# Performance work log

Measured on AMD Instinct MI355X. Metric: run time of the kernel, lower is better.

## Reference

```python
import jax, jax.numpy as jnp
import numpy as np


def setup_inputs() -> dict:
    key = jax.random.key(0)
    k1, k2 = jax.random.split(key)
    input_tensor = jax.random.normal(k1, (32, 128, 64, 64), dtype=jnp.float32)
    weights = jax.random.normal(k2, (256, 128, 3, 3), dtype=jnp.float32) * 0.05
    return {"input_tensor": input_tensor, "weights": weights}


def reference(input_tensor, weights):
    # Valid-padding, stride-1, no-bias direct conv2d (NCHW x OIHW -> NCHW),
    # identical math to the quintuple-loop slice*weight sum in the original.
    return jax.lax.conv_general_dilated(
        input_tensor,
        weights,
        window_strides=(1, 1),
        padding="VALID",
        dimension_numbers=("NCHW", "OIHW", "NCHW"),
    )
```

## Files before the change

kernel.cpp:

```cpp
#include <hip/hip_runtime.h>
#include <hip/hip_bf16.h>

#define N_IMG 32
#define CIN   128
#define INH   64
#define INW   64
#define COUT  256
#define OH    62
#define OW    62

typedef short          bf16x8 __attribute__((ext_vector_type(8)));
typedef unsigned short u16x8  __attribute__((ext_vector_type(8)));
typedef float          f32x4  __attribute__((ext_vector_type(4)));

__device__ __forceinline__ unsigned short f2bf(float x) {
    unsigned int u = __float_as_uint(x);
    u += 0x7fffu + ((u >> 16) & 1u);
    return (unsigned short)(u >> 16);
}

__global__ void wt_transform_kernel(const float* __restrict__ Wsrc,
                                    unsigned short* __restrict__ WT) {
    int idx = blockIdx.x * 256 + threadIdx.x;
    int i   = idx & 7;
    int co  = (idx >> 3) & 255;
    int cgk = idx >> 11;
    int cg  = cgk & 15;
    int khw = cgk >> 4;
    int kh  = khw / 3, kw = khw - 3 * kh;
    int ci  = cg * 8 + i;
    WT[idx] = f2bf(Wsrc[co * (CIN * 9) + ci * 9 + kh * 3 + kw]);
}

__global__ __launch_bounds__(256, 2)
void conv_mfma_kernel(const float* __restrict__ In,
                      const unsigned short* __restrict__ WT,
                      float* __restrict__ Out) {
    __shared__ unsigned short Lin[66 * 32];

    const int oh   = blockIdx.x;
    const int img  = blockIdx.y;
    const int tid  = threadIdx.x;
    const int wave = tid >> 6;
    const int lane = tid & 63;
    const int q    = lane >> 4;
    const int ml   = lane & 15;
    const int co_base = wave * 64;

    f32x4 acc[4][4];
    const f32x4 zero = {0.f, 0.f, 0.f, 0.f};
#pragma unroll
    for (int a = 0; a < 4; ++a)
#pragma unroll
        for (int b = 0; b < 4; ++b) acc[a][b] = zero;

    if (tid < 32) ((unsigned int*)&Lin[64 * 32])[tid] = 0u;

    const int s_iw = tid & 63;
    const int s_cg = tid >> 6;
    const bf16x8* WTv = (const bf16x8*)WT;

    for (int kh = 0; kh < 3; ++kh) {
        const int ih = oh + kh;
        for (int cb = 0; cb < 4; ++cb) {
            const float* p = In + (((img * CIN + cb * 32 + s_cg * 8) * INH + ih) * INW + s_iw);
            u16x8 v;
#pragma unroll
            for (int i = 0; i < 8; ++i) v[i] = f2bf(p[i * (INH * INW)]);
            __syncthreads();
            *(u16x8*)&Lin[s_iw * 32 + ((s_cg ^ (s_iw & 3)) << 3)] = v;
            __syncthreads();

#pragma unroll
            for (int kw = 0; kw < 3; ++kw) {
                const int khw = kh * 3 + kw;
                bf16x8 wf[4], xf[4];
#pragma unroll
                for (int mi = 0; mi < 4; ++mi)
                    wf[mi] = WTv[(khw * 16 + cb * 4 + q) * 256 + co_base + mi * 16 + ml];
#pragma unroll
                for (int ni = 0; ni < 4; ++ni) {
                    const int row = ni * 16 + ml + kw;
                    xf[ni] = *(const bf16x8*)&Lin[row * 32 + ((q ^ (row & 3)) << 3)];
                }
#pragma unroll
                for (int mi = 0; mi < 4; ++mi)
#pragma unroll
                    for (int ni = 0; ni < 4; ++ni)
                        acc[mi][ni] = __builtin_amdgcn_mfma_f32_16x16x32_bf16(
                            wf[mi], xf[ni], acc[mi][ni], 0, 0, 0);
            }
        }
    }

#pragma unroll
    for (int mi = 0; mi < 4; ++mi) {
#pragma unroll
        for (int r = 0; r < 4; ++r) {
            const int co = co_base + mi * 16 + q * 4 + r;
            float* op = Out + ((img * COUT + co) * OH + oh) * OW;
#pragma unroll
            for (int ni = 0; ni < 4; ++ni) {
                const int ow = ni * 16 + ml;
                if (ow < OW) op[ow] = acc[mi][ni][r];
            }
        }
    }
}

__global__ void conv_naive_kernel(const float* __restrict__ In,
                                  const float* __restrict__ Wt,
                                  float* __restrict__ Out) {
    int idx = blockIdx.x * 256 + threadIdx.x;
    const int total = N_IMG * COUT * OH * OW;
    if (idx >= total) return;
    int ow = idx % OW; int t = idx / OW;
    int oh = t % OH;   t /= OH;
    int co = t % COUT; int img = t / COUT;
    float s = 0.f;
    for (int ci = 0; ci < CIN; ++ci)
#pragma unroll
        for (int kh = 0; kh < 3; ++kh)
#pragma unroll
            for (int kw = 0; kw < 3; ++kw)
                s += In[((img * CIN + ci) * INH + oh + kh) * INW + ow + kw] *
                     Wt[co * CIN * 9 + ci * 9 + kh * 3 + kw];
    Out[idx] = s;
}

extern "C" void kernel_launch(void* const* d_in, const int* in_sizes, int n_in,
                              void* d_out, int out_size, void* d_ws, size_t ws_size,
                              hipStream_t stream) {
    const float* In   = (const float*)d_in[0];
    const float* Wsrc = (const float*)d_in[1];
    float* Out        = (float*)d_out;

    const size_t WT_BYTES = (size_t)9 * 16 * 256 * 8 * sizeof(unsigned short);
    if (ws_size >= WT_BYTES) {
        unsigned short* WT = (unsigned short*)d_ws;
        wt_transform_kernel<<<dim3(294912 / 256), dim3(256), 0, stream>>>(Wsrc, WT);
        conv_mfma_kernel<<<dim3(OH, N_IMG), dim3(256), 0, stream>>>(In, WT, Out);
    } else {
        const int total = N_IMG * COUT * OH * OW;
        conv_naive_kernel<<<dim3((total + 255) / 256), dim3(256), 0, stream>>>(In, Wsrc, Out);
    }
}
```

Baseline: 240.5 us.

## Pre-convert input to swizzled bf16 and double-buffer it into LDS via direct loads

Adds a separate kernel that converts the fp32 NCHW input once into a bf16, channel-blocked, XOR-swizzled layout in workspace. The conv kernel then streams rows straight into LDS with global_load_lds, double-buffered so the next stage loads while MFMAs run on the current one. It also halves threads per block, giving each wave 128 output channels, and remaps block ids to spread work. The aim is to remove repeated fp32 loads and conversions of each input row from the main loop and to hide load latency. The cost is an extra kernel launch and a full-tensor bf16 write and read through workspace, plus a path that only runs when the workspace is large enough.

```diff
diff --git a/kernel.cpp b/kernel.cpp
--- a/kernel.cpp
+++ b/kernel.cpp
@@ -17,6 +17,12 @@
     unsigned int u = __float_as_uint(x);
     u += 0x7fffu + ((u >> 16) & 1u);
     return (unsigned short)(u >> 16);
+}
+
+__device__ __forceinline__ void gload_lds16(const void* g, void* l) {
+    __builtin_amdgcn_global_load_lds(
+        (const __attribute__((address_space(1))) unsigned int*)g,
+        (__attribute__((address_space(3))) unsigned int*)l, 16, 0, 0);
 }
 
 __global__ void wt_transform_kernel(const float* __restrict__ Wsrc,
@@ -32,10 +38,121 @@
     WT[idx] = f2bf(Wsrc[co * (CIN * 9) + ci * 9 + kh * 3 + kw]);
 }
 
+__global__ __launch_bounds__(256)
+void in_transform_kernel(const float* __restrict__ In,
+                         unsigned short* __restrict__ TIn) {
+    const int bid = blockIdx.x;
+    const int ih  = bid & 63;
+    const int cb  = (bid >> 6) & 3;
+    const int img = bid >> 8;
+    const int c   = threadIdx.x;
+    const int iw  = c >> 2;
+    const int cg  = (c & 3) ^ ((iw >> 1) & 3);
+    const float* p = In + ((img * CIN + cb * 32 + cg * 8) * INH + ih) * INW + iw;
+    u16x8 v;
+#pragma unroll
+    for (int i = 0; i < 8; ++i) v[i] = f2bf(p[i * (INH * INW)]);
+    *(u16x8*)&TIn[(bid * 256 + c) * 8] = v;
+}
+
+__global__ __launch_bounds__(128, 2)
+void conv_mfma_bf16_kernel(const unsigned short* __restrict__ TIn,
+                           const unsigned short* __restrict__ WT,
+                           float* __restrict__ Out) {
+    __shared__ unsigned short Lin[2][2112];
+
+    const int g   = blockIdx.x;
+    const int f   = (g & 7) * 248 + (g >> 3);
+    const int img = f / OH;
+    const int oh  = f - img * OH;
+
+    const int tid  = threadIdx.x;
+    const int wave = tid >> 6;
+    const int lane = tid & 63;
+    const int q    = lane >> 4;
+    const int ml   = lane & 15;
+    const int co_base = wave * 128;
+
+    const unsigned short* tin_base = TIn + (size_t)img * (4 * 64 * 2048);
+    const bf16x8* WTv = (const bf16x8*)WT;
+    const int wlane = q * 256 + co_base + ml;
+
+    int xoff[3][4];
+#pragma unroll
+    for (int kw = 0; kw < 3; ++kw)
+#pragma unroll
+        for (int ni = 0; ni < 4; ++ni) {
+            const int r = ni * 16 + ml + kw;
+            xoff[kw][ni] = r * 32 + ((q ^ ((r >> 1) & 3)) << 3);
+        }
+
+    f32x4 acc[8][4];
+    const f32x4 zero = {0.f, 0.f, 0.f, 0.f};
+#pragma unroll
+    for (int a = 0; a < 8; ++a)
+#pragma unroll
+        for (int b = 0; b < 4; ++b) acc[a][b] = zero;
+
+    {
+        const unsigned short* src = tin_base + (oh) * 2048;
+        gload_lds16(src + (wave * 64 + lane) * 8, &Lin[0][wave * 512]);
+        gload_lds16(src + (128 + wave * 64 + lane) * 8, &Lin[0][1024 + wave * 512]);
+    }
+    if (tid < 64) ((unsigned int*)&Lin[tid >> 5][64 * 32])[tid & 31] = 0u;
+    __syncthreads();
+
+    for (int s = 0; s < 12; ++s) {
+        const int cur = s & 1;
+        if (s < 11) {
+            const int s1 = s + 1;
+            const unsigned short* src =
+                tin_base + ((s1 & 3) * 64 + oh + (s1 >> 2)) * 2048;
+            gload_lds16(src + (wave * 64 + lane) * 8, &Lin[cur ^ 1][wave * 512]);
+            gload_lds16(src + (128 + wave * 64 + lane) * 8,
+                        &Lin[cur ^ 1][1024 + wave * 512]);
+        }
+        const int kh = s >> 2, cb = s & 3;
+#pragma unroll
+        for (int kw = 0; kw < 3; ++kw) {
+            const int khw = kh * 3 + kw;
+            const bf16x8* wbase = WTv + (khw * 16 + cb * 4) * 256;
+            bf16x8 wf[8];
+#pragma unroll
+            for (int mi = 0; mi < 8; ++mi)
+                wf[mi] = wbase[wlane + mi * 16];
+            bf16x8 xf[4];
+#pragma unroll
+            for (int ni = 0; ni < 4; ++ni)
+                xf[ni] = *(const bf16x8*)&Lin[cur][xoff[kw][ni]];
+#pragma unroll
+            for (int mi = 0; mi < 8; ++mi)
+#pragma unroll
+                for (int ni = 0; ni < 4; ++ni)
+                    acc[mi][ni] = __builtin_amdgcn_mfma_f32_16x16x32_bf16(
+                        wf[mi], xf[ni], acc[mi][ni], 0, 0, 0);
+        }
+        __syncthreads();
+    }
+
+#pragma unroll
+    for (int mi = 0; mi < 8; ++mi) {
+#pragma unroll
+        for (int r = 0; r < 4; ++r) {
+            const int co = co_base + mi * 16 + q * 4 + r;
+            float* op = Out + ((img * COUT + co) * OH + oh) * OW;
+#pragma unroll
+            for (int ni = 0; ni < 4; ++ni) {
+                const int ow = ni * 16 + ml;
+                if (ow < OW) op[ow] = acc[mi][ni][r];
+            }
+        }
+    }
+}
+
 __global__ __launch_bounds__(256, 2)
-void conv_mfma_kernel(const float* __restrict__ In,
-                      const unsigned short* __restrict__ WT,
-                      float* __restrict__ Out) {
+void conv_mfma_fp32_kernel(const float* __restrict__ In,
+                           const unsigned short* __restrict__ WT,
+                           float* __restrict__ Out) {
     __shared__ unsigned short Lin[66 * 32];
 
     const int oh   = blockIdx.x;
@@ -135,11 +252,19 @@
     const float* Wsrc = (const float*)d_in[1];
     float* Out        = (float*)d_out;
 
-    const size_t WT_BYTES = (size_t)9 * 16 * 256 * 8 * sizeof(unsigned short);
-    if (ws_size >= WT_BYTES) {
+    const size_t WT_BYTES  = (size_t)9 * 16 * 256 * 8 * sizeof(unsigned short);
+    const size_t TIN_BYTES = (size_t)N_IMG * 4 * 64 * 2048 * sizeof(unsigned short);
+
+    if (ws_size >= WT_BYTES + TIN_BYTES) {
+        unsigned short* WT  = (unsigned short*)d_ws;
+        unsigned short* TIn = (unsigned short*)((char*)d_ws + WT_BYTES);
+        wt_transform_kernel<<<dim3(294912 / 256), dim3(256), 0, stream>>>(Wsrc, WT);
+        in_transform_kernel<<<dim3(N_IMG * 4 * 64), dim3(256), 0, stream>>>(In, TIn);
+        conv_mfma_bf16_kernel<<<dim3(OH * N_IMG), dim3(128), 0, stream>>>(TIn, WT, Out);
+    } else if (ws_size >= WT_BYTES) {
         unsigned short* WT = (unsigned short*)d_ws;
         wt_transform_kernel<<<dim3(294912 / 256), dim3(256), 0, stream>>>(Wsrc, WT);
-        conv_mfma_kernel<<<dim3(OH, N_IMG), dim3(256), 0, stream>>>(In, WT, Out);
+        conv_mfma_fp32_kernel<<<dim3(OH, N_IMG), dim3(256), 0, stream>>>(In, WT, Out);
     } else {
         const int total = N_IMG * COUT * OH * OW;
         conv_naive_kernel<<<dim3((total + 255) / 256), dim3(256), 0, stream>>>(In, Wsrc, Out);
```

Result: slower. 365.4 us (+51.9%).
